# Optimization experiments

Hardware: AMD Instinct MI355X
Metric: run time of the kernel (lower is better)

The kernel has to match this reference:

```python
import jax, jax.numpy as jnp
import numpy as np

EPS = 1e-5  # torch layer_norm / group_norm default eps

def _ln(x, w):
    mu = x.mean(-1, keepdims=True)
    var = x.var(-1, keepdims=True)
    return (x - mu) / jnp.sqrt(var + EPS) * w

def _mh_ln(x, w, nh):
    # MultiHeadLayerNorm == group_norm with nh groups over last dim, weight, no bias
    B, S, D = x.shape
    xh = x.reshape(B, S, nh, D // nh)
    mu = xh.mean(-1, keepdims=True)
    var = xh.var(-1, keepdims=True)
    return ((xh - mu) / jnp.sqrt(var + EPS)).reshape(B, S, D) * w

def _causal_conv(x, k, b):
    # depthwise causal conv1d, x: (B,S,C), k: (C,K)
    K = k.shape[1]
    S = x.shape[1]
    xp = jnp.pad(x, ((0, 0), (K - 1, 0), (0, 0)))
    y = sum(xp[:, i:i + S, :] * k[:, i] for i in range(K))
    return y + b

def _headwise(x, W):
    # LinearHeadwiseExpand: block-diagonal linear, W: (nh, out_per_head, in_per_head)
    B, S, D = x.shape
    nh, o, i = W.shape
    xh = x.reshape(B, S, nh, i)
    return jnp.einsum('bshi,hoi->bsho', xh, W).reshape(B, S, nh * o)

def _mlstm_parallel(q, k, v, ig, fg, eps=1e-6):
    # q,k,v: (B,NH,S,DH); ig,fg: (B,NH,S) gate preactivations
    B, NH, S, DH = q.shape
    logf = jax.nn.log_sigmoid(fg)
    lc = jnp.cumsum(logf, axis=-1)
    # log_fg_matrix[t,s] = sum_{j=s+1..t} log sigmoid(f_j)
    lfm = lc[..., :, None] - lc[..., None, :]
    mask = jnp.tril(jnp.ones((S, S), dtype=bool))
    logD = jnp.where(mask, lfm + ig[..., None, :], -jnp.inf)
    maxD = jnp.max(logD, axis=-1, keepdims=True)
    D = jnp.exp(logD - maxD)
    qk = jnp.einsum('bhsd,bhtd->bhst', q, k) / jnp.sqrt(jnp.float32(DH))
    C = qk * D
    normalizer = jnp.maximum(jnp.abs(C.sum(-1, keepdims=True)), jnp.exp(-maxD))
    return jnp.einsum('bhst,bhtd->bhsd', C / (normalizer + eps), v)

def _slstm_scan(gx, R, b):
    # gx: (B,S,NH,4,DH) input-gate preacts (i,f,z,o); R: (NH,DH,4,DH); b: (NH,4,DH)
    B, S, NH, G, DH = gx.shape
    gx_t = jnp.moveaxis(gx, 1, 0)
    z0 = jnp.zeros((B, NH, DH), gx.dtype)
    def step(carry, inp):
        y, c, n, m = carry
        g, t = inp
        raw = g + jnp.einsum('bhd,hdge->bhge', y, R) + b
        iraw, fraw, zraw, oraw = raw[:, :, 0], raw[:, :, 1], raw[:, :, 2], raw[:, :, 3]
        logfplusm = m + jax.nn.log_sigmoid(fraw)
        mnew = jnp.where(t == 0, iraw, jnp.maximum(iraw, logfplusm))
        og = jax.nn.sigmoid(oraw)
        ig = jnp.exp(iraw - mnew)
        fg = jnp.exp(logfplusm - mnew)
        cnew = fg * c + ig * jnp.tanh(zraw)
        nnew = fg * n + ig
        ynew = og * cnew / nnew
        return (ynew, cnew, nnew, mnew), ynew
    _, ys = jax.lax.scan(step, (z0, z0, z0, z0), (gx_t, jnp.arange(S)))
    return jnp.moveaxis(ys, 0, 1)  # (B,S,NH,DH)

def _forward(x, W_in, b_in, ln0_w, m_Wup, m_bup, m_convk, m_convb, m_Wq, m_bq, m_Wk, m_bk, m_Wv, m_bv, m_Wig, m_big, m_Wfg, m_bfg, m_onw, m_skip, m_Wd, m_bd, ln1_w, s_convk, s_convb, s_Wi, s_Wf, s_Wz, s_Wo, s_R, s_b, s_gnw, ffn_nw, f_Wu, f_bu, f_Wd, f_bd, post_w, fc_W, fc_b):
    B, S, _ = x.shape
    NH, DH = 4, 64  # mLSTM heads
    h = x @ W_in.T + b_in  # input_proj (dropout is identity in eval)
    # ---- block 0: mLSTM (pre-norm residual) ----
    r = _ln(h, ln0_w)
    up = r @ m_Wup.T + m_bup
    xm, z = jnp.split(up, 2, axis=-1)  # (B,S,256) each
    xc = jax.nn.silu(_causal_conv(xm, m_convk, m_convb))
    q = _headwise(xc, m_Wq) + m_bq
    k = _headwise(xc, m_Wk) + m_bk
    v = _headwise(xm, m_Wv) + m_bv
    qkv = jnp.concatenate([q, k, v], axis=-1)  # (B,S,768)
    igp = (qkv @ m_Wig.T + m_big).transpose(0, 2, 1)  # (B,NH,S)
    fgp = (qkv @ m_Wfg.T + m_bfg).transpose(0, 2, 1)
    qh = q.reshape(B, S, NH, DH).transpose(0, 2, 1, 3)
    kh = k.reshape(B, S, NH, DH).transpose(0, 2, 1, 3)
    vh = v.reshape(B, S, NH, DH).transpose(0, 2, 1, 3)
    hc = _mlstm_parallel(qh, kh, vh, igp, fgp)
    hc = hc.transpose(0, 2, 1, 3).reshape(B, S, NH * DH)
    ht = _mh_ln(hc, m_onw, NH)
    hs = (ht + m_skip * xc) * jax.nn.silu(z)
    h = h + hs @ m_Wd.T + m_bd
    # ---- block 1: sLSTM (pre-norm residual) ----
    SNH, SDH = 4, 32
    r = _ln(h, ln1_w)
    rc = jax.nn.silu(_causal_conv(r, s_convk, s_convb))
    gi = _headwise(rc, s_Wi).reshape(B, S, SNH, SDH)
    gf = _headwise(rc, s_Wf).reshape(B, S, SNH, SDH)
    gz = _headwise(r, s_Wz).reshape(B, S, SNH, SDH)
    go = _headwise(r, s_Wo).reshape(B, S, SNH, SDH)
    gx = jnp.stack([gi, gf, gz, go], axis=3)  # (B,S,NH,4,DH)
    ys = _slstm_scan(gx, s_R, s_b).reshape(B, S, SNH * SDH)
    h = h + _mh_ln(ys, s_gnw, SNH)
    # gated feedforward (gelu)
    r = _ln(h, ffn_nw)
    u = r @ f_Wu.T + f_bu
    g, u2 = jnp.split(u, 2, axis=-1)
    h = h + (jax.nn.gelu(g, approximate=False) * u2) @ f_Wd.T + f_bd
    hp = _ln(h, post_w)
    return hp[:, -1, :] @ fc_W.T + fc_b

def setup_inputs() -> dict:
    key = jax.random.key(0)
    ks = iter(jax.random.split(key, 64))
    def rn(shape, scale=1.0):
        return jax.random.normal(next(ks), shape, dtype=jnp.float32) * scale
    B, S, F, D = 8, 1024, 75, 128
    inner = 256
    return dict(
        x=rn((B, S, F)),
        W_in=rn((D, F), F ** -0.5), b_in=rn((D,), 0.02),
        ln0_w=jnp.ones((D,), jnp.float32),
        m_Wup=rn((2 * inner, D), D ** -0.5), m_bup=rn((2 * inner,), 0.02),
        m_convk=rn((inner, 4), 0.5), m_convb=rn((inner,), 0.02),
        m_Wq=rn((64, 4, 4), 0.5), m_bq=rn((inner,), 0.02),
        m_Wk=rn((64, 4, 4), 0.5), m_bk=rn((inner,), 0.02),
        m_Wv=rn((64, 4, 4), 0.5), m_bv=rn((inner,), 0.02),
        m_Wig=rn((4, 3 * inner), (3 * inner) ** -0.5), m_big=rn((4,), 0.1),
        m_Wfg=rn((4, 3 * inner), (3 * inner) ** -0.5), m_bfg=rn((4,), 0.1) + 3.0,
        m_onw=jnp.ones((inner,), jnp.float32),
        m_skip=jnp.ones((inner,), jnp.float32),
        m_Wd=rn((D, inner), inner ** -0.5), m_bd=rn((D,), 0.02),
        ln1_w=jnp.ones((D,), jnp.float32),
        s_convk=rn((D, 4), 0.5), s_convb=rn((D,), 0.02),
        s_Wi=rn((4, 32, 32), 32 ** -0.5),
        s_Wf=rn((4, 32, 32), 32 ** -0.5),
        s_Wz=rn((4, 32, 32), 32 ** -0.5),
        s_Wo=rn((4, 32, 32), 32 ** -0.5),
        s_R=rn((4, 32, 4, 32), 32 ** -0.5),
        s_b=rn((4, 4, 32), 0.1),
        s_gnw=jnp.ones((D,), jnp.float32),
        ffn_nw=jnp.ones((D,), jnp.float32),
        f_Wu=rn((384, D), D ** -0.5), f_bu=rn((384,), 0.02),
        f_Wd=rn((D, 192), 192 ** -0.5), f_bd=rn((D,), 0.02),
        post_w=jnp.ones((D,), jnp.float32),
        fc_W=rn((1, D), D ** -0.5), fc_b=rn((1,), 0.02),
    )

def reference(x, W_in, b_in, ln0_w, m_Wup, m_bup, m_convk, m_convb, m_Wq, m_bq, m_Wk, m_bk, m_Wv, m_bv, m_Wig, m_big, m_Wfg, m_bfg, m_onw, m_skip, m_Wd, m_bd, ln1_w, s_convk, s_convb, s_Wi, s_Wf, s_Wz, s_Wo, s_R, s_b, s_gnw, ffn_nw, f_Wu, f_bu, f_Wd, f_bd, post_w, fc_W, fc_b):
    return _forward(x, W_in, b_in, ln0_w, m_Wup, m_bup, m_convk, m_convb, m_Wq, m_bq, m_Wk, m_bk, m_Wv, m_bv, m_Wig, m_big, m_Wfg, m_bfg, m_onw, m_skip, m_Wd, m_bd, ln1_w, s_convk, s_convb, s_Wi, s_Wf, s_Wz, s_Wo, s_R, s_b, s_gnw, ffn_nw, f_Wu, f_bu, f_Wd, f_bd, post_w, fc_W, fc_b)
```

## Files before the change

### kernel.cpp

```cpp
#include <hip/hip_runtime.h>
#include <hip/hip_bf16.h>
#include <math.h>

#define B_ 8
#define S_ 1024
#define F_ 75
#define D_ 128
#define INNER_ 256
#define NH_ 4
#define DH_ 64
#define MROWS_ (B_*S_)

static __device__ __forceinline__ float frcp(float x){ return __builtin_amdgcn_rcpf(x); }
static __device__ __forceinline__ float fsigm(float x){ return frcp(1.0f + __expf(-x)); }
static __device__ __forceinline__ float flogsig(float x){
    return fminf(x, 0.f) - __logf(1.0f + __expf(-fabsf(x)));
}
static __device__ __forceinline__ float ftanh(float z){
    return 1.0f - 2.0f*frcp(__expf(2.0f*z) + 1.0f);
}

__global__ __launch_bounds__(256, 2) void gemm_bias_big(
        const float* __restrict__ A, const float* __restrict__ W,
        const float* __restrict__ bias, const float* __restrict__ res,
        float* __restrict__ C, int M, int N, int K) {
    __shared__ float As[64*68];
    __shared__ float Ws[64*68];
    int tid = threadIdx.x;
    int wid = tid >> 6, lane = tid & 63;
    int wy = wid >> 1, wx = wid & 1;
    int sg = lane >> 3, tg = lane & 7;
    int m0 = blockIdx.y*64, n0 = blockIdx.x*64;
    int r = tid >> 2, c0 = (tid & 3) << 4;
    bool vec = ((K & 3) == 0);
    float acc[4][4];
    #pragma unroll
    for (int i = 0; i < 4; ++i)
        #pragma unroll
        for (int j = 0; j < 4; ++j) acc[i][j] = 0.f;

    for (int k0 = 0; k0 < K; k0 += 64) {
        __syncthreads();
        const float* Ar = A + (size_t)(m0+r)*K + k0;
        const float* Wr = W + (size_t)(n0+r)*K + k0;
        if (vec) {
            #pragma unroll
            for (int i = 0; i < 4; ++i) {
                *(float4*)(&As[r*68 + c0 + 4*i]) = *(const float4*)(Ar + c0 + 4*i);
                *(float4*)(&Ws[r*68 + c0 + 4*i]) = *(const float4*)(Wr + c0 + 4*i);
            }
        } else {
            #pragma unroll
            for (int i = 0; i < 4; ++i)
                #pragma unroll
                for (int e = 0; e < 4; ++e) {
                    int c = c0 + 4*i + e;
                    bool ok = (k0 + c) < K;
                    As[r*68 + c] = ok ? Ar[c] : 0.f;
                    Ws[r*68 + c] = ok ? Wr[c] : 0.f;
                }
        }
        __syncthreads();
        const float* arow = &As[(32*wy + sg)*68];
        const float* brow = &Ws[(32*wx + tg)*68];
        #pragma unroll 2
        for (int d = 0; d < 64; d += 4) {
            float4 b0 = *(const float4*)(brow + 0*544 + d);
            float4 b1 = *(const float4*)(brow + 1*544 + d);
            float4 b2 = *(const float4*)(brow + 2*544 + d);
            float4 b3 = *(const float4*)(brow + 3*544 + d);
            #pragma unroll
            for (int i = 0; i < 4; ++i) {
                float4 a = *(const float4*)(arow + i*544 + d);
                acc[i][0] += a.x*b0.x + a.y*b0.y + a.z*b0.z + a.w*b0.w;
                acc[i][1] += a.x*b1.x + a.y*b1.y + a.z*b1.z + a.w*b1.w;
                acc[i][2] += a.x*b2.x + a.y*b2.y + a.z*b2.z + a.w*b2.w;
                acc[i][3] += a.x*b3.x + a.y*b3.y + a.z*b3.z + a.w*b3.w;
            }
        }
    }
    #pragma unroll
    for (int i = 0; i < 4; ++i) {
        int m = m0 + 32*wy + 8*i + sg;
        #pragma unroll
        for (int j = 0; j < 4; ++j) {
            int n = n0 + 32*wx + 8*j + tg;
            float v = acc[i][j] + bias[n];
            if (res) v += res[(size_t)m*N + n];
            C[(size_t)m*N + n] = v;
        }
    }
}

__global__ void ln_kernel(const float* __restrict__ X, const float* __restrict__ w,
                          float* __restrict__ Y) {
    int row = blockIdx.x, t = threadIdx.x;
    float v = X[(size_t)row*128 + t];
    __shared__ float s1[128], s2[128];
    s1[t]=v; s2[t]=v*v; __syncthreads();
    for (int off=64; off>0; off>>=1){
        if (t<off){ s1[t]+=s1[t+off]; s2[t]+=s2[t+off]; }
        __syncthreads();
    }
    float mu = s1[0]*(1.f/128.f);
    float var = s2[0]*(1.f/128.f) - mu*mu;
    Y[(size_t)row*128 + t] = (v-mu)*rsqrtf(var+1e-5f)*w[t];
}

__global__ __launch_bounds__(64) void mlstm_qkv(
        const float* __restrict__ up, const float* __restrict__ convk,
        const float* __restrict__ convb,
        const float* __restrict__ Wq, const float* __restrict__ bq,
        const float* __restrict__ Wk, const float* __restrict__ bk,
        const float* __restrict__ Wv, const float* __restrict__ bv,
        const float* __restrict__ Wig, const float* __restrict__ big,
        const float* __restrict__ Wfg, const float* __restrict__ bfg,
        float* __restrict__ xc, float* __restrict__ q, float* __restrict__ k,
        float* __restrict__ v, float* __restrict__ igp, float* __restrict__ fgp) {
    int row = blockIdx.x;
    int b = row >> 10, s = row & 1023;
    int l = threadIdx.x;
    int c0 = l*4;
    float4 xm[4];
    #pragma unroll
    for (int i = 0; i < 4; ++i) {
        int sp = s - 3 + i;
        if (sp >= 0) xm[i] = *(const float4*)(up + (size_t)(row-3+i)*512 + c0);
        else         xm[i] = make_float4(0.f,0.f,0.f,0.f);
    }
    float xcv[4];
    #pragma unroll
    for (int j = 0; j < 4; ++j) {
        int c = c0 + j;
        float acc = convb[c];
        #pragma unroll
        for (int i = 0; i < 4; ++i)
            acc += ((const float*)&xm[i])[j] * convk[c*4+i];
        xcv[j] = acc * fsigm(acc);
    }
    *(float4*)(xc + (size_t)row*256 + c0) = make_float4(xcv[0],xcv[1],xcv[2],xcv[3]);
    float qv[4], kv[4], vv[4];
    #pragma unroll
    for (int o = 0; o < 4; ++o) {
        const float* wq = Wq + ((size_t)l*4 + o)*4;
        const float* wk = Wk + ((size_t)l*4 + o)*4;
        const float* wv = Wv + ((size_t)l*4 + o)*4;
        float aq = bq[c0+o], ak = bk[c0+o], avv = bv[c0+o];
        #pragma unroll
        for (int i = 0; i < 4; ++i) {
            aq  += xcv[i]*wq[i];
            ak  += xcv[i]*wk[i];
            avv += ((const float*)&xm[3])[i]*wv[i];
        }
        qv[o]=aq; kv[o]=ak; vv[o]=avv;
    }
    *(float4*)(q + (size_t)row*256 + c0) = make_float4(qv[0],qv[1],qv[2],qv[3]);
    *(float4*)(k + (size_t)row*256 + c0) = make_float4(kv[0],kv[1],kv[2],kv[3]);
    *(float4*)(v + (size_t)row*256 + c0) = make_float4(vv[0],vv[1],vv[2],vv[3]);
    float dots[8];
    #pragma unroll
    for (int g = 0; g < 4; ++g) {
        float di = 0.f, df = 0.f;
        #pragma unroll
        for (int j = 0; j < 4; ++j) {
            di += qv[j]*Wig[g*768 + c0 + j] + kv[j]*Wig[g*768 + 256 + c0 + j]
                + vv[j]*Wig[g*768 + 512 + c0 + j];
            df += qv[j]*Wfg[g*768 + c0 + j] + kv[j]*Wfg[g*768 + 256 + c0 + j]
                + vv[j]*Wfg[g*768 + 512 + c0 + j];
        }
        dots[g] = di; dots[4+g] = df;
    }
    #pragma unroll
    for (int off = 32; off > 0; off >>= 1)
        #pragma unroll
        for (int g = 0; g < 8; ++g) dots[g] += __shfl_down(dots[g], off, 64);
    if (l == 0) {
        #pragma unroll
        for (int g = 0; g < 4; ++g) {
            igp[((size_t)b*NH_+g)*S_ + s] = dots[g]   + big[g];
            fgp[((size_t)b*NH_+g)*S_ + s] = dots[4+g] + bfg[g];
        }
    }
}

__global__ __launch_bounds__(128) void slstm_convgates(
        const float* __restrict__ r, const float* __restrict__ convk,
        const float* __restrict__ convb, const float* __restrict__ Wi,
        const float* __restrict__ Wf, const float* __restrict__ Wz,
        const float* __restrict__ Wo, float* __restrict__ GX) {
    int row = blockIdx.x; int s = row & 1023;
    int c = threadIdx.x;
    __shared__ float rcL[128], rL[128];
    float rv = r[(size_t)row*128 + c];
    float acc = convb[c];
    #pragma unroll
    for (int i = 0; i < 4; ++i) {
        int sp = s - 3 + i;
        if (sp >= 0) acc += r[(size_t)(row-3+i)*128 + c]*convk[c*4+i];
    }
    float rcv = acc * fsigm(acc);
    rcL[c] = rcv; rL[c] = rv;
    __syncthreads();
    int h = c >> 5, o = c & 31;
    size_t wb = ((size_t)h*32 + o)*32;
    const float* rc_ = rcL + h*32;
    const float* rr_ = rL + h*32;
    float di=0.f, df=0.f, dz=0.f, doo=0.f;
    #pragma unroll
    for (int i = 0; i < 32; ++i) {
        float a = rc_[i], cc = rr_[i];
        di  += a*Wi[wb+i];
        df  += a*Wf[wb+i];
        dz  += cc*Wz[wb+i];
        doo += cc*Wo[wb+i];
    }
    float* g = GX + (size_t)row*512 + h*128 + o;
    g[0]  = di;
    g[32] = df;
    g[64] = dz;
    g[96] = doo;
}

__global__ void mlstm_scan_pre(const float* __restrict__ igp, const float* __restrict__ fgp,
                               float* __restrict__ lc, float* __restrict__ av,
                               float* __restrict__ mx) {
    int bh = blockIdx.x; int t = threadIdx.x;
    __shared__ float buf[2][1024];
    float ls = flogsig(fgp[(size_t)bh*S_ + t]);
    int cur = 0;
    buf[0][t] = ls; __syncthreads();
    for (int off=1; off<1024; off<<=1) {
        float x2 = buf[cur][t];
        if (t >= off) x2 += buf[cur][t-off];
        buf[cur^1][t] = x2; cur ^= 1; __syncthreads();
    }
    float lcv = buf[cur][t];
    lc[(size_t)bh*S_+t] = lcv;
    float a = igp[(size_t)bh*S_+t] - lcv;
    av[(size_t)bh*S_+t] = a;
    __syncthreads();
    cur = 0; buf[0][t] = a; __syncthreads();
    for (int off=1; off<1024; off<<=1) {
        float x2 = buf[cur][t];
        if (t >= off) x2 = fmaxf(x2, buf[cur][t-off]);
        buf[cur^1][t] = x2; cur ^= 1; __syncthreads();
    }
    mx[(size_t)bh*S_+t] = buf[cur][t];
}

__global__ __launch_bounds__(256, 2) void mlstm_attn_tiled(
        const float* __restrict__ q, const float* __restrict__ k,
        const float* __restrict__ v, const float* __restrict__ lc,
        const float* __restrict__ av, const float* __restrict__ mx,
        float* __restrict__ hc) {
    int bid = blockIdx.x;
    int stile = 15 - (bid & 15);
    int bh = bid >> 4;
    int hh = bh & 3, b = bh >> 2;
    int s0 = stile << 6;
    int tid = threadIdx.x;
    int wid = tid >> 6, lane = tid & 63;
    int wy = wid >> 1, wx = wid & 1;
    int sg = lane >> 3, tg = lane & 7;

    __shared__ float qs[64*68];
    __shared__ float kst[64*68];
    __shared__ float vtT[64*68];
    __shared__ float avt[64], maxsL[64], normL[64], rsumL[128];

    const size_t bhS = (size_t)bh * S_;
    {
        int r = tid >> 2, c0 = (tid & 3) << 4;
        const float* qg = q + ((size_t)(b*S_) + s0 + r)*INNER_ + hh*64;
        #pragma unroll
        for (int i = 0; i < 4; ++i) {
            float4 t4 = *(const float4*)(qg + c0 + 4*i);
            float4 w4; w4.x=t4.x*0.125f; w4.y=t4.y*0.125f; w4.z=t4.z*0.125f; w4.w=t4.w*0.125f;
            *(float4*)(&qs[r*68 + c0 + 4*i]) = w4;
        }
        if (tid < 64) maxsL[tid] = lc[bhS + s0 + tid] + mx[bhS + s0 + tid];
    }
    float msv[4];
    #pragma unroll
    for (int i = 0; i < 4; ++i)
        msv[i] = mx[bhS + s0 + 32*wy + 8*i + sg];

    float O[4][4];
    float rsAcc[4];
    #pragma unroll
    for (int i = 0; i < 4; ++i) {
        rsAcc[i] = 0.f;
        #pragma unroll
        for (int j = 0; j < 4; ++j) O[i][j] = 0.f;
    }

    for (int t0 = 0; t0 <= s0; t0 += 64) {
        __syncthreads();
        {
            int r = tid >> 2, c0 = (tid & 3) << 4;
            const float* kg = k + ((size_t)(b*S_) + t0 + r)*INNER_ + hh*64;
            const float* vg = v + ((size_t)(b*S_) + t0 + r)*INNER_ + hh*64;
            #pragma unroll
            for (int i = 0; i < 4; ++i) {
                *(float4*)(&kst[r*68 + c0 + 4*i]) = *(const float4*)(kg + c0 + 4*i);
                float4 v4 = *(const float4*)(vg + c0 + 4*i);
                int dc = c0 + 4*i;
                vtT[(dc+0)*68 + r] = v4.x;
                vtT[(dc+1)*68 + r] = v4.y;
                vtT[(dc+2)*68 + r] = v4.z;
                vtT[(dc+3)*68 + r] = v4.w;
            }
            if (tid < 64) avt[tid] = av[bhS + t0 + tid];
        }
        __syncthreads();
        float dot[4][4];
        #pragma unroll
        for (int i = 0; i < 4; ++i)
            #pragma unroll
            for (int j = 0; j < 4; ++j) dot[i][j] = 0.f;
        {
            const float* qrow = &qs[(32*wy + sg)*68];
            const float* krow = &kst[(32*wx + tg)*68];
            #pragma unroll 2
            for (int d = 0; d < 64; d += 4) {
                float4 b0 = *(const float4*)(krow + 0*544 + d);
                float4 b1 = *(const float4*)(krow + 1*544 + d);
                float4 b2 = *(const float4*)(krow + 2*544 + d);
                float4 b3 = *(const float4*)(krow + 3*544 + d);
                #pragma unroll
                for (int i = 0; i < 4; ++i) {
                    float4 a = *(const float4*)(qrow + i*544 + d);
                    dot[i][0] += a.x*b0.x + a.y*b0.y + a.z*b0.z + a.w*b0.w;
                    dot[i][1] += a.x*b1.x + a.y*b1.y + a.z*b1.z + a.w*b1.w;
                    dot[i][2] += a.x*b2.x + a.y*b2.y + a.z*b2.z + a.w*b2.w;
                    dot[i][3] += a.x*b3.x + a.y*b3.y + a.z*b3.z + a.w*b3.w;
                }
            }
        }
        __syncthreads();
        #pragma unroll
        for (int i = 0; i < 4; ++i) {
            int s_loc = 32*wy + 8*i + sg;
            float rp = 0.f;
            #pragma unroll
            for (int j = 0; j < 4; ++j) {
                int t_loc = 32*wx + 8*j + tg;
                bool ok = (t0 + t_loc) <= (s0 + s_loc);
                float p = ok ? dot[i][j]*__expf(avt[t_loc] - msv[i]) : 0.f;
                kst[s_loc*68 + t_loc] = p;
                rp += p;
            }
            rp += __shfl_xor(rp, 1);
            rp += __shfl_xor(rp, 2);
            rp += __shfl_xor(rp, 4);
            rsAcc[i] += rp;
        }
        __syncthreads();
        {
            const float* prow = &kst[(32*wy + sg)*68];
            const float* vrow = &vtT[(32*wx + tg)*68];
            #pragma unroll 2
            for (int tt = 0; tt < 64; tt += 4) {
                float4 b0 = *(const float4*)(vrow + 0*544 + tt);
                float4 b1 = *(const float4*)(vrow + 1*544 + tt);
                float4 b2 = *(const float4*)(vrow + 2*544 + tt);
                float4 b3 = *(const float4*)(vrow + 3*544 + tt);
                #pragma unroll
                for (int i = 0; i < 4; ++i) {
                    float4 a = *(const float4*)(prow + i*544 + tt);
                    O[i][0] += a.x*b0.x + a.y*b0.y + a.z*b0.z + a.w*b0.w;
                    O[i][1] += a.x*b1.x + a.y*b1.y + a.z*b1.z + a.w*b1.w;
                    O[i][2] += a.x*b2.x + a.y*b2.y + a.z*b2.z + a.w*b2.w;
                    O[i][3] += a.x*b3.x + a.y*b3.y + a.z*b3.z + a.w*b3.w;
                }
            }
        }
    }
    if (tg == 0) {
        #pragma unroll
        for (int i = 0; i < 4; ++i)
            rsumL[wx*64 + 32*wy + 8*i + sg] = rsAcc[i];
    }
    __syncthreads();
    if (tid < 64) {
        float tot = rsumL[tid] + rsumL[64 + tid];
        normL[tid] = fmaxf(fabsf(tot), __expf(-maxsL[tid])) + 1e-6f;
    }
    __syncthreads();
    #pragma unroll
    for (int i = 0; i < 4; ++i) {
        int s_loc = 32*wy + 8*i + sg;
        float inv = 1.0f / normL[s_loc];
        #pragma unroll
        for (int j = 0; j < 4; ++j) {
            int d_loc = 32*wx + 8*j + tg;
            hc[((size_t)(b*S_) + s0 + s_loc)*INNER_ + hh*64 + d_loc] = O[i][j] * inv;
        }
    }
}

__global__ void mlstm_out(const float* __restrict__ hc, const float* __restrict__ xc,
                          const float* __restrict__ up, const float* __restrict__ onw,
                          const float* __restrict__ skip, float* __restrict__ hs) {
    int row = blockIdx.x; int c = threadIdx.x;
    float v = hc[(size_t)row*INNER_ + c];
    __shared__ float s1[256], s2[256];
    s1[c]=v; s2[c]=v*v; __syncthreads();
    int li = c & 63;
    for (int off=32; off>0; off>>=1){
        if (li < off){ s1[c]+=s1[c+off]; s2[c]+=s2[c+off]; }
        __syncthreads();
    }
    int base = c & ~63;
    float mu = s1[base]*(1.f/64.f);
    float var = s2[base]*(1.f/64.f) - mu*mu;
    float ht = (v-mu)*rsqrtf(var+1e-5f)*onw[c];
    float z = up[(size_t)row*512 + 256 + c];
    hs[(size_t)row*INNER_ + c] = (ht + skip[c]*xc[(size_t)row*INNER_+c]) * (z*fsigm(z));
}

__global__ __launch_bounds__(64, 1) void slstm_scan_wave(
        const float* __restrict__ gx, const float* __restrict__ R,
        const float* __restrict__ bb, float* __restrict__ ys) {
    int blk = blockIdx.x; int hh = blk & 3; int b = blk >> 2;
    int l = threadIdx.x;
    int e = l >> 1, p = l & 1;
    int o0 = p*32 + e, o1 = (p+2)*32 + e;
    float Rc0[32], Rc1[32];
    #pragma unroll
    for (int d = 0; d < 32; ++d) {
        Rc0[d] = R[(size_t)(hh*32 + d)*128 + o0];
        Rc1[d] = R[(size_t)(hh*32 + d)*128 + o1];
        asm volatile("" : "+v"(Rc0[d]));
        asm volatile("" : "+v"(Rc1[d]));
    }
    float bj0 = bb[hh*128 + o0], bj1 = bb[hh*128 + o1];
    float cst = 0.f, nst = 0.f, mst = 0.f, y = 0.f;
    const float* gbase = gx + (size_t)(b*S_)*512 + hh*128;
    float* ybase = ys + (size_t)(b*S_)*128 + hh*32 + e;
    float ga[4], gb[4];
    #pragma unroll
    for (int u = 0; u < 4; ++u) {
        ga[u] = gbase[(size_t)u*512 + o0];
        gb[u] = gbase[(size_t)u*512 + o1];
    }
    for (int t = 0; t < S_; t += 4) {
        float gna[4], gnb[4];
        #pragma unroll
        for (int u = 0; u < 4; ++u) {
            int tn = t + 4 + u;
            size_t off = (size_t)(tn < S_ ? tn : 0) * 512;
            gna[u] = gbase[off + o0];
            gnb[u] = gbase[off + o1];
        }
        #pragma unroll
        for (int u = 0; u < 4; ++u) {
            float a0=0.f, a1=0.f, a2=0.f, a3=0.f;
            float c0=0.f, c1=0.f, c2=0.f, c3=0.f;
            #pragma unroll
            for (int d = 0; d < 32; d += 4) {
                float y0 = __int_as_float(__builtin_amdgcn_readlane(__float_as_int(y), 2*d));
                float y1 = __int_as_float(__builtin_amdgcn_readlane(__float_as_int(y), 2*d+2));
                float y2 = __int_as_float(__builtin_amdgcn_readlane(__float_as_int(y), 2*d+4));
                float y3 = __int_as_float(__builtin_amdgcn_readlane(__float_as_int(y), 2*d+6));
                a0 += y0*Rc0[d];   c0 += y0*Rc1[d];
                a1 += y1*Rc0[d+1]; c1 += y1*Rc1[d+1];
                a2 += y2*Rc0[d+2]; c2 += y2*Rc1[d+2];
                a3 += y3*Rc0[d+3]; c3 += y3*Rc1[d+3];
            }
            float r0 = ga[u] + bj0 + ((a0+a1)+(a2+a3));
            float r1 = gb[u] + bj1 + ((c0+c1)+(c2+c3));
            float fo0 = __int_as_float(__builtin_amdgcn_mov_dpp(__float_as_int(r0), 0xB1, 0xF, 0xF, true));
            float fo1 = __int_as_float(__builtin_amdgcn_mov_dpp(__float_as_int(r1), 0xB1, 0xF, 0xF, true));
            float iraw = p ? fo0 : r0;
            float fraw = p ? r0 : fo0;
            float zraw = p ? fo1 : r1;
            float oraw = p ? r1 : fo1;
            int t_abs = t + u;
            float lfm = mst + flogsig(fraw);
            float mnew = (t_abs == 0) ? iraw : fmaxf(iraw, lfm);
            float igv = __expf(iraw - mnew), fgv = __expf(lfm - mnew);
            cst = fgv*cst + igv*ftanh(zraw);
            nst = fgv*nst + igv;
            mst = mnew;
            y = cst * frcp(nst * (1.0f + __expf(-oraw)));
            if (p == 0) ybase[(size_t)t_abs*128] = y;
        }
        #pragma unroll
        for (int u = 0; u < 4; ++u) { ga[u] = gna[u]; gb[u] = gnb[u]; }
    }
}

__global__ void slstm_addnorm_ln(const float* __restrict__ ys, const float* __restrict__ gnw,
                                 const float* __restrict__ ffnw,
                                 float* __restrict__ h, float* __restrict__ r) {
    int row = blockIdx.x; int c = threadIdx.x;
    __shared__ float s1[128], s2[128];
    float v = ys[(size_t)row*128 + c];
    s1[c]=v; s2[c]=v*v; __syncthreads();
    int li = c & 31;
    for (int off=16; off>0; off>>=1){
        if (li < off){ s1[c]+=s1[c+off]; s2[c]+=s2[c+off]; }
        __syncthreads();
    }
    int base = c & ~31;
    float mu = s1[base]*(1.f/32.f);
    float var = s2[base]*(1.f/32.f) - mu*mu;
    float hn = h[(size_t)row*128 + c] + (v-mu)*rsqrtf(var+1e-5f)*gnw[c];
    h[(size_t)row*128 + c] = hn;
    __syncthreads();
    s1[c]=hn; s2[c]=hn*hn; __syncthreads();
    for (int off=64; off>0; off>>=1){
        if (c<off){ s1[c]+=s1[c+off]; s2[c]+=s2[c+off]; }
        __syncthreads();
    }
    float mu2 = s1[0]*(1.f/128.f);
    float var2 = s2[0]*(1.f/128.f) - mu2*mu2;
    r[(size_t)row*128 + c] = (hn-mu2)*rsqrtf(var2+1e-5f)*ffnw[c];
}

__global__ void ffn_act(const float* __restrict__ u, float* __restrict__ act) {
    int idx = blockIdx.x*blockDim.x + threadIdx.x;
    int total = MROWS_*192;
    if (idx >= total) return;
    int j = idx % 192; int m = idx / 192;
    float g  = u[(size_t)m*384 + j];
    float u2 = u[(size_t)m*384 + 192 + j];
    float ge = 0.5f*g*(1.0f + erff(g*0.70710678118f));
    act[(size_t)m*192 + j] = ge*u2;
}

__global__ void final_ln_fc(const float* __restrict__ h, const float* __restrict__ postw,
                            const float* __restrict__ fcW, const float* __restrict__ fcb,
                            float* __restrict__ out) {
    int b = blockIdx.x; int t = threadIdx.x;
    const float* hr = h + (size_t)(b*S_ + S_-1)*128;
    float v = hr[t];
    __shared__ float s1[128], s2[128];
    s1[t]=v; s2[t]=v*v; __syncthreads();
    for (int off=64; off>0; off>>=1){
        if (t<off){ s1[t]+=s1[t+off]; s2[t]+=s2[t+off]; }
        __syncthreads();
    }
    float mu = s1[0]*(1.f/128.f);
    float var = s2[0]*(1.f/128.f) - mu*mu;
    float hp = (v-mu)*rsqrtf(var+1e-5f)*postw[t];
    __syncthreads();
    s1[t] = hp*fcW[t]; __syncthreads();
    for (int off=64; off>0; off>>=1){
        if (t<off) s1[t]+=s1[t+off];
        __syncthreads();
    }
    if (t == 0) out[b] = s1[0] + fcb[0];
}

extern "C" void kernel_launch(void* const* d_in, const int* in_sizes, int n_in,
                              void* d_out, int out_size, void* d_ws, size_t ws_size,
                              hipStream_t stream) {
    const float* x       = (const float*)d_in[0];
    const float* W_in    = (const float*)d_in[1];
    const float* b_in    = (const float*)d_in[2];
    const float* ln0_w   = (const float*)d_in[3];
    const float* m_Wup   = (const float*)d_in[4];
    const float* m_bup   = (const float*)d_in[5];
    const float* m_convk = (const float*)d_in[6];
    const float* m_convb = (const float*)d_in[7];
    const float* m_Wq    = (const float*)d_in[8];
    const float* m_bq    = (const float*)d_in[9];
    const float* m_Wk    = (const float*)d_in[10];
    const float* m_bk    = (const float*)d_in[11];
    const float* m_Wv    = (const float*)d_in[12];
    const float* m_bv    = (const float*)d_in[13];
    const float* m_Wig   = (const float*)d_in[14];
    const float* m_big   = (const float*)d_in[15];
    const float* m_Wfg   = (const float*)d_in[16];
    const float* m_bfg   = (const float*)d_in[17];
    const float* m_onw   = (const float*)d_in[18];
    const float* m_skip  = (const float*)d_in[19];
    const float* m_Wd    = (const float*)d_in[20];
    const float* m_bd    = (const float*)d_in[21];
    const float* ln1_w   = (const float*)d_in[22];
    const float* s_convk = (const float*)d_in[23];
    const float* s_convb = (const float*)d_in[24];
    const float* s_Wi    = (const float*)d_in[25];
    const float* s_Wf    = (const float*)d_in[26];
    const float* s_Wz    = (const float*)d_in[27];
    const float* s_Wo    = (const float*)d_in[28];
    const float* s_R     = (const float*)d_in[29];
    const float* s_b     = (const float*)d_in[30];
    const float* s_gnw   = (const float*)d_in[31];
    const float* ffn_nw  = (const float*)d_in[32];
    const float* f_Wu    = (const float*)d_in[33];
    const float* f_bu    = (const float*)d_in[34];
    const float* f_Wd    = (const float*)d_in[35];
    const float* f_bd    = (const float*)d_in[36];
    const float* post_w  = (const float*)d_in[37];
    const float* fc_W    = (const float*)d_in[38];
    const float* fc_b    = (const float*)d_in[39];
    float* out = (float*)d_out;

    float* W = (float*)d_ws;
    const size_t M1 = 1048576;
    float* h    = W;
    float* r    = W + 1*M1;
    float* up   = W + 2*M1;
    float* xc   = W + 6*M1;
    float* q    = W + 8*M1;
    float* kbuf = W + 10*M1;
    float* vbuf = W + 12*M1;
    float* hc   = W + 14*M1;
    float* igp  = W + 16*M1;
    float* fgp  = igp + 32768;
    float* lc   = fgp + 32768;
    float* av   = lc  + 32768;
    float* mx   = av  + 32768;
    float* hs   = q;
    float* gx   = kbuf;
    float* ys   = hc;
    float* u    = up;
    float* act  = q;

    gemm_bias_big<<<dim3(128/64, MROWS_/64), 256, 0, stream>>>(x, W_in, b_in, nullptr, h, MROWS_, 128, F_);
    ln_kernel<<<MROWS_, 128, 0, stream>>>(h, ln0_w, r);
    gemm_bias_big<<<dim3(512/64, MROWS_/64), 256, 0, stream>>>(r, m_Wup, m_bup, nullptr, up, MROWS_, 512, 128);
    mlstm_qkv<<<MROWS_, 64, 0, stream>>>(up, m_convk, m_convb, m_Wq, m_bq, m_Wk, m_bk,
                                         m_Wv, m_bv, m_Wig, m_big, m_Wfg, m_bfg,
                                         xc, q, kbuf, vbuf, igp, fgp);
    mlstm_scan_pre<<<B_*NH_, 1024, 0, stream>>>(igp, fgp, lc, av, mx);
    mlstm_attn_tiled<<<B_*NH_*16, 256, 0, stream>>>(q, kbuf, vbuf, lc, av, mx, hc);
    mlstm_out<<<MROWS_, 256, 0, stream>>>(hc, xc, up, m_onw, m_skip, hs);
    gemm_bias_big<<<dim3(128/64, MROWS_/64), 256, 0, stream>>>(hs, m_Wd, m_bd, h, h, MROWS_, 128, 256);
    ln_kernel<<<MROWS_, 128, 0, stream>>>(h, ln1_w, r);
    slstm_convgates<<<MROWS_, 128, 0, stream>>>(r, s_convk, s_convb, s_Wi, s_Wf, s_Wz, s_Wo, gx);
    slstm_scan_wave<<<B_*NH_, 64, 0, stream>>>(gx, s_R, s_b, ys);
    slstm_addnorm_ln<<<MROWS_, 128, 0, stream>>>(ys, s_gnw, ffn_nw, h, r);
    gemm_bias_big<<<dim3(384/64, MROWS_/64), 256, 0, stream>>>(r, f_Wu, f_bu, nullptr, u, MROWS_, 384, 128);
    ffn_act<<<(MROWS_*192)/256, 256, 0, stream>>>(u, act);
    gemm_bias_big<<<dim3(128/64, MROWS_/64), 256, 0, stream>>>(act, f_Wd, f_bd, h, h, MROWS_, 128, 192);
    final_ln_fc<<<B_, 128, 0, stream>>>(h, post_w, fc_W, fc_b, out);
    (void)in_sizes; (void)n_in; (void)out_size; (void)ws_size;
}
```

Measured before the change: 915.6 us.

## Fuse layernorm into GEMM epilogues and GELU gating into FFN up-projection

Adds a gemm_ln kernel whose blocks each own 64 full rows of the 128-wide output, so they can compute the residual add, row mean and variance, and layernorm in the epilogue. This replaces the separate ln_kernel launches and their extra read of h. A second kernel, gemm_ffn_act, computes the gate and up halves of the FFN projection together and applies GELU times up before storing, so the 384-wide intermediate never goes to memory and the ffn_act launch is dropped. In exchange, the gemm_ln grid drops to 128 blocks, which may leave many CUs idle, and both kernels need more shared memory and registers.

After: 941.8 us. 1.03x slower.

```diff
diff --git a/kernel.cpp b/kernel.cpp
--- a/kernel.cpp
+++ b/kernel.cpp
@@ -92,19 +92,192 @@
     }
 }
 
-__global__ void ln_kernel(const float* __restrict__ X, const float* __restrict__ w,
-                          float* __restrict__ Y) {
-    int row = blockIdx.x, t = threadIdx.x;
-    float v = X[(size_t)row*128 + t];
-    __shared__ float s1[128], s2[128];
-    s1[t]=v; s2[t]=v*v; __syncthreads();
-    for (int off=64; off>0; off>>=1){
-        if (t<off){ s1[t]+=s1[t+off]; s2[t]+=s2[t+off]; }
-        __syncthreads();
-    }
-    float mu = s1[0]*(1.f/128.f);
-    float var = s2[0]*(1.f/128.f) - mu*mu;
-    Y[(size_t)row*128 + t] = (v-mu)*rsqrtf(var+1e-5f)*w[t];
+__global__ __launch_bounds__(256, 2) void gemm_ln(
+        const float* __restrict__ A, const float* __restrict__ W,
+        const float* __restrict__ bias, const float* __restrict__ res,
+        const float* __restrict__ lnw, float* __restrict__ H,
+        float* __restrict__ Rout, int M, int K) {
+    __shared__ float As[64*68];
+    __shared__ float Ws[128*68];
+    __shared__ float Lsum[2][64], Lssq[2][64];
+    int tid = threadIdx.x;
+    int wid = tid >> 6, lane = tid & 63;
+    int wy = wid >> 1, wx = wid & 1;
+    int sg = lane >> 3, tg = lane & 7;
+    int m0 = blockIdx.x*64;
+    int r = tid >> 2, c0 = (tid & 3) << 4;
+    int rw = tid >> 1, cw0 = (tid & 1) << 5;
+    bool vec = ((K & 3) == 0);
+    float acc[4][8];
+    #pragma unroll
+    for (int i = 0; i < 4; ++i)
+        #pragma unroll
+        for (int j = 0; j < 8; ++j) acc[i][j] = 0.f;
+
+    for (int k0 = 0; k0 < K; k0 += 64) {
+        __syncthreads();
+        const float* Ar = A + (size_t)(m0+r)*K + k0;
+        const float* Wr = W + (size_t)rw*K + k0;
+        if (vec) {
+            #pragma unroll
+            for (int i = 0; i < 4; ++i)
+                *(float4*)(&As[r*68 + c0 + 4*i]) = *(const float4*)(Ar + c0 + 4*i);
+            #pragma unroll
+            for (int i = 0; i < 8; ++i)
+                *(float4*)(&Ws[rw*68 + cw0 + 4*i]) = *(const float4*)(Wr + cw0 + 4*i);
+        } else {
+            #pragma unroll
+            for (int i = 0; i < 4; ++i)
+                #pragma unroll
+                for (int e = 0; e < 4; ++e) {
+                    int c = c0 + 4*i + e;
+                    As[r*68 + c] = ((k0 + c) < K) ? Ar[c] : 0.f;
+                }
+            #pragma unroll
+            for (int i = 0; i < 8; ++i)
+                #pragma unroll
+                for (int e = 0; e < 4; ++e) {
+                    int c = cw0 + 4*i + e;
+                    Ws[rw*68 + c] = ((k0 + c) < K) ? Wr[c] : 0.f;
+                }
+        }
+        __syncthreads();
+        const float* arow = &As[(32*wy + sg)*68];
+        const float* brow = &Ws[(64*wx + tg)*68];
+        #pragma unroll 1
+        for (int d = 0; d < 64; d += 4) {
+            float4 bv[8];
+            #pragma unroll
+            for (int j = 0; j < 8; ++j)
+                bv[j] = *(const float4*)(brow + j*544 + d);
+            #pragma unroll
+            for (int i = 0; i < 4; ++i) {
+                float4 a = *(const float4*)(arow + i*544 + d);
+                #pragma unroll
+                for (int j = 0; j < 8; ++j)
+                    acc[i][j] += a.x*bv[j].x + a.y*bv[j].y + a.z*bv[j].z + a.w*bv[j].w;
+            }
+        }
+    }
+    float ps[4], pss[4];
+    #pragma unroll
+    for (int i = 0; i < 4; ++i) {
+        int m = m0 + 32*wy + 8*i + sg;
+        float s = 0.f, ss = 0.f;
+        #pragma unroll
+        for (int j = 0; j < 8; ++j) {
+            int n = 64*wx + 8*j + tg;
+            float vv = acc[i][j] + bias[n];
+            if (res) vv += res[(size_t)m*128 + n];
+            acc[i][j] = vv;
+            s += vv; ss += vv*vv;
+        }
+        ps[i] = s; pss[i] = ss;
+    }
+    #pragma unroll
+    for (int bm = 1; bm <= 4; bm <<= 1)
+        #pragma unroll
+        for (int i = 0; i < 4; ++i) {
+            ps[i]  += __shfl_xor(ps[i],  bm, 64);
+            pss[i] += __shfl_xor(pss[i], bm, 64);
+        }
+    if (tg == 0) {
+        #pragma unroll
+        for (int i = 0; i < 4; ++i) {
+            int rloc = 32*wy + 8*i + sg;
+            Lsum[wx][rloc] = ps[i];
+            Lssq[wx][rloc] = pss[i];
+        }
+    }
+    __syncthreads();
+    #pragma unroll
+    for (int i = 0; i < 4; ++i) {
+        int rloc = 32*wy + 8*i + sg;
+        int m = m0 + rloc;
+        float s  = Lsum[0][rloc] + Lsum[1][rloc];
+        float ss = Lssq[0][rloc] + Lssq[1][rloc];
+        float mu = s*(1.f/128.f);
+        float var = ss*(1.f/128.f) - mu*mu;
+        float inv = rsqrtf(var + 1e-5f);
+        #pragma unroll
+        for (int j = 0; j < 8; ++j) {
+            int n = 64*wx + 8*j + tg;
+            float vv = acc[i][j];
+            H[(size_t)m*128 + n]    = vv;
+            Rout[(size_t)m*128 + n] = (vv-mu)*inv*lnw[n];
+        }
+    }
+}
+
+__global__ __launch_bounds__(256, 2) void gemm_ffn_act(
+        const float* __restrict__ A, const float* __restrict__ Wu,
+        const float* __restrict__ bu, float* __restrict__ act, int M) {
+    __shared__ float As[64*68];
+    __shared__ float Wg[64*68];
+    __shared__ float Wu2[64*68];
+    int tid = threadIdx.x;
+    int wid = tid >> 6, lane = tid & 63;
+    int wy = wid >> 1, wx = wid & 1;
+    int sg = lane >> 3, tg = lane & 7;
+    int m0 = blockIdx.y*64, nb = blockIdx.x*64;
+    int r = tid >> 2, c0 = (tid & 3) << 4;
+    float ag[4][4], au[4][4];
+    #pragma unroll
+    for (int i = 0; i < 4; ++i)
+        #pragma unroll
+        for (int j = 0; j < 4; ++j) { ag[i][j] = 0.f; au[i][j] = 0.f; }
+
+    for (int k0 = 0; k0 < 128; k0 += 64) {
+        __syncthreads();
+        const float* Ar = A + (size_t)(m0+r)*128 + k0;
+        const float* Wgr = Wu + (size_t)(nb+r)*128 + k0;
+        const float* Wur = Wu + (size_t)(192+nb+r)*128 + k0;
+        #pragma unroll
+        for (int i = 0; i < 4; ++i) {
+            *(float4*)(&As[r*68 + c0 + 4*i])  = *(const float4*)(Ar + c0 + 4*i);
+            *(float4*)(&Wg[r*68 + c0 + 4*i])  = *(const float4*)(Wgr + c0 + 4*i);
+            *(float4*)(&Wu2[r*68 + c0 + 4*i]) = *(const float4*)(Wur + c0 + 4*i);
+        }
+        __syncthreads();
+        const float* arow = &As[(32*wy + sg)*68];
+        const float* grow = &Wg[(32*wx + tg)*68];
+        const float* urow = &Wu2[(32*wx + tg)*68];
+        #pragma unroll 2
+        for (int d = 0; d < 64; d += 4) {
+            float4 g0 = *(const float4*)(grow + 0*544 + d);
+            float4 g1 = *(const float4*)(grow + 1*544 + d);
+            float4 g2 = *(const float4*)(grow + 2*544 + d);
+            float4 g3 = *(const float4*)(grow + 3*544 + d);
+            float4 u0 = *(const float4*)(urow + 0*544 + d);
+            float4 u1 = *(const float4*)(urow + 1*544 + d);
+            float4 u2 = *(const float4*)(urow + 2*544 + d);
+            float4 u3 = *(const float4*)(urow + 3*544 + d);
+            #pragma unroll
+            for (int i = 0; i < 4; ++i) {
+                float4 a = *(const float4*)(arow + i*544 + d);
+                ag[i][0] += a.x*g0.x + a.y*g0.y + a.z*g0.z + a.w*g0.w;
+                ag[i][1] += a.x*g1.x + a.y*g1.y + a.z*g1.z + a.w*g1.w;
+                ag[i][2] += a.x*g2.x + a.y*g2.y + a.z*g2.z + a.w*g2.w;
+                ag[i][3] += a.x*g3.x + a.y*g3.y + a.z*g3.z + a.w*g3.w;
+                au[i][0] += a.x*u0.x + a.y*u0.y + a.z*u0.z + a.w*u0.w;
+                au[i][1] += a.x*u1.x + a.y*u1.y + a.z*u1.z + a.w*u1.w;
+                au[i][2] += a.x*u2.x + a.y*u2.y + a.z*u2.z + a.w*u2.w;
+                au[i][3] += a.x*u3.x + a.y*u3.y + a.z*u3.z + a.w*u3.w;
+            }
+        }
+    }
+    #pragma unroll
+    for (int i = 0; i < 4; ++i) {
+        int m = m0 + 32*wy + 8*i + sg;
+        #pragma unroll
+        for (int j = 0; j < 4; ++j) {
+            int n = nb + 32*wx + 8*j + tg;
+            float g  = ag[i][j] + bu[n];
+            float u2 = au[i][j] + bu[192+n];
+            float ge = 0.5f*g*(1.0f + erff(g*0.70710678118f));
+            act[(size_t)m*192 + n] = ge*u2;
+        }
+    }
 }
 
 __global__ __launch_bounds__(64) void mlstm_qkv(
@@ -517,17 +690,6 @@
     float mu2 = s1[0]*(1.f/128.f);
     float var2 = s2[0]*(1.f/128.f) - mu2*mu2;
     r[(size_t)row*128 + c] = (hn-mu2)*rsqrtf(var2+1e-5f)*ffnw[c];
-}
-
-__global__ void ffn_act(const float* __restrict__ u, float* __restrict__ act) {
-    int idx = blockIdx.x*blockDim.x + threadIdx.x;
-    int total = MROWS_*192;
-    if (idx >= total) return;
-    int j = idx % 192; int m = idx / 192;
-    float g  = u[(size_t)m*384 + j];
-    float u2 = u[(size_t)m*384 + 192 + j];
-    float ge = 0.5f*g*(1.0f + erff(g*0.70710678118f));
-    act[(size_t)m*192 + j] = ge*u2;
 }
 
 __global__ void final_ln_fc(const float* __restrict__ h, const float* __restrict__ postw,
@@ -617,11 +779,9 @@
     float* hs   = q;
     float* gx   = kbuf;
     float* ys   = hc;
-    float* u    = up;
     float* act  = q;
 
-    gemm_bias_big<<<dim3(128/64, MROWS_/64), 256, 0, stream>>>(x, W_in, b_in, nullptr, h, MROWS_, 128, F_);
-    ln_kernel<<<MROWS_, 128, 0, stream>>>(h, ln0_w, r);
+    gemm_ln<<<MROWS_/64, 256, 0, stream>>>(x, W_in, b_in, nullptr, ln0_w, h, r, MROWS_, F_);
     gemm_bias_big<<<dim3(512/64, MROWS_/64), 256, 0, stream>>>(r, m_Wup, m_bup, nullptr, up, MROWS_, 512, 128);
     mlstm_qkv<<<MROWS_, 64, 0, stream>>>(up, m_convk, m_convb, m_Wq, m_bq, m_Wk, m_bk,
                                          m_Wv, m_bv, m_Wig, m_big, m_Wfg, m_bfg,
@@ -629,13 +789,11 @@
     mlstm_scan_pre<<<B_*NH_, 1024, 0, stream>>>(igp, fgp, lc, av, mx);
     mlstm_attn_tiled<<<B_*NH_*16, 256, 0, stream>>>(q, kbuf, vbuf, lc, av, mx, hc);
     mlstm_out<<<MROWS_, 256, 0, stream>>>(hc, xc, up, m_onw, m_skip, hs);
-    gemm_bias_big<<<dim3(128/64, MROWS_/64), 256, 0, stream>>>(hs, m_Wd, m_bd, h, h, MROWS_, 128, 256);
-    ln_kernel<<<MROWS_, 128, 0, stream>>>(h, ln1_w, r);
+    gemm_ln<<<MROWS_/64, 256, 0, stream>>>(hs, m_Wd, m_bd, h, ln1_w, h, r, MROWS_, 256);
     slstm_convgates<<<MROWS_, 128, 0, stream>>>(r, s_convk, s_convb, s_Wi, s_Wf, s_Wz, s_Wo, gx);
     slstm_scan_wave<<<B_*NH_, 64, 0, stream>>>(gx, s_R, s_b, ys);
     slstm_addnorm_ln<<<MROWS_, 128, 0, stream>>>(ys, s_gnw, ffn_nw, h, r);
-    gemm_bias_big<<<dim3(384/64, MROWS_/64), 256, 0, stream>>>(r, f_Wu, f_bu, nullptr, u, MROWS_, 384, 128);
-    ffn_act<<<(MROWS_*192)/256, 256, 0, stream>>>(u, act);
+    gemm_ffn_act<<<dim3(3, MROWS_/64), 256, 0, stream>>>(r, f_Wu, f_bu, act, MROWS_);
     gemm_bias_big<<<dim3(128/64, MROWS_/64), 256, 0, stream>>>(act, f_Wd, f_bd, h, h, MROWS_, 128, 192);
     final_ln_fc<<<B_, 128, 0, stream>>>(h, post_w, fc_W, fc_b, out);
     (void)in_sizes; (void)n_in; (void)out_size; (void)ws_size;
```
